# Kernel tuning notes

Measured on AMD Instinct MI355X. Metric: run time of the kernel, lower is better.

Reference implementation:

```python
import jax, jax.numpy as jnp
import numpy as np

EPS = 1e-12  # torch F.normalize default eps

def _l2norm(x):
    # torch.nn.functional.normalize(x, dim=-1): x / max(||x||_2, eps)
    n = jnp.linalg.norm(x, axis=-1, keepdims=True)
    return x / jnp.maximum(n, EPS)

def setup_inputs() -> dict:
    key = jax.random.key(0)
    ks = jax.random.split(key, 12)
    B, T, D, V, C = 16, 2048, 1024, 32000, 6
    s = 0.02
    text = jax.random.randint(ks[0], (B * T,), 0, V, dtype=jnp.int64)
    offsets = (jnp.arange(B, dtype=jnp.int64) * T)  # uniform-length sequences
    emb = jax.random.normal(ks[1], (V, D), dtype=jnp.float32) * s
    Wq = jax.random.normal(ks[2], (D, D), dtype=jnp.float32) * s
    bq = jnp.zeros((D,), jnp.float32)
    Wk = jax.random.normal(ks[3], (D, D), dtype=jnp.float32) * s
    bk = jnp.zeros((D,), jnp.float32)
    Wv = jax.random.normal(ks[4], (D, D), dtype=jnp.float32) * s
    bv = jnp.zeros((D,), jnp.float32)
    Wfc = jax.random.normal(ks[5], (D, D), dtype=jnp.float32) * s
    bfc = jnp.zeros((D,), jnp.float32)
    Wo = jax.random.normal(ks[6], (C, D), dtype=jnp.float32) * s
    bo = jnp.zeros((C,), jnp.float32)
    return {"text": text, "offsets": offsets, "emb": emb,
            "Wq": Wq, "bq": bq, "Wk": Wk, "bk": bk, "Wv": Wv, "bv": bv,
            "Wfc": Wfc, "bfc": bfc, "Wo": Wo, "bo": bo}

def reference(text, offsets, emb, Wq, bq, Wk, bk, Wv, bv, Wfc, bfc, Wo, bo):
    B = offsets.shape[0]
    T = text.shape[0] // B  # uniform lengths -> pad_sequence == reshape
    D = emb.shape[1]
    tok = text.reshape(B, T)
    x = emb[tok]                                   # [B,T,D]
    q = x @ Wq.T + bq
    k = x @ Wk.T + bk
    v = x @ Wv.T + bv
    scores = jnp.einsum('bqd,bkd->bqk', q, k) / jnp.sqrt(jnp.asarray(D, x.dtype))
    causal = jnp.tril(jnp.ones((T, T), dtype=bool))
    scores = jnp.where(causal[None, :, :], scores, -jnp.inf)
    attn = jax.nn.softmax(scores, axis=-1)
    out = jnp.einsum('bqk,bkd->bqd', attn, v) + x  # residual with embedding
    out = _l2norm(out)
    out = out + (out @ Wfc.T + bfc)                # residual FFN
    out = _l2norm(out)
    last = out[:, -1, :]                           # [B,D]
    return jax.nn.sigmoid(last @ Wo.T + bo)        # [B,num_class]
```

## Files before the change

### kernel.cpp

```cpp
#include <hip/hip_runtime.h>
#include <math.h>


typedef unsigned short ushort_t;

__device__ __forceinline__ float bf2f(ushort_t u) {
    union { unsigned int i; float f; } v;
    v.i = ((unsigned int)u) << 16;
    return v.f;
}

__device__ __forceinline__ ushort_t f2bf(float f) {
    union { float f; unsigned int i; } v; v.f = f;
    unsigned int lsb = (v.i >> 16) & 1;
    unsigned int r = v.i + 0x7FFF + lsb;
    return (ushort_t)(r >> 16);
}

__device__ __forceinline__ float wave_sum(float acc) {
    #pragma unroll
    for (int off = 32; off >= 1; off >>= 1) acc += __shfl_xor(acc, off, 64);
    return acc;
}
__device__ __forceinline__ float wave_max(float acc) {
    #pragma unroll
    for (int off = 32; off >= 1; off >>= 1) acc = fmaxf(acc, __shfl_xor(acc, off, 64));
    return acc;
}

__device__ __forceinline__ void ld8(const void* p, int isbf, size_t i, float* o) {
    if (isbf) {
        uint4 raw = *reinterpret_cast<const uint4*>((const ushort_t*)p + i);
        const ushort_t* pu = reinterpret_cast<const ushort_t*>(&raw);
        #pragma unroll
        for (int k = 0; k < 8; ++k) o[k] = bf2f(pu[k]);
    } else {
        const float4* f = reinterpret_cast<const float4*>((const float*)p + i);
        float4 a = f[0], b = f[1];
        o[0]=a.x; o[1]=a.y; o[2]=a.z; o[3]=a.w;
        o[4]=b.x; o[5]=b.y; o[6]=b.z; o[7]=b.w;
    }
}

__device__ __forceinline__ void ld4(const void* p, int isbf, size_t i, float* o) {
    if (isbf) {
        uint2 raw = *reinterpret_cast<const uint2*>((const ushort_t*)p + i);
        const ushort_t* pu = reinterpret_cast<const ushort_t*>(&raw);
        #pragma unroll
        for (int k = 0; k < 4; ++k) o[k] = bf2f(pu[k]);
    } else {
        float4 a = *reinterpret_cast<const float4*>((const float*)p + i);
        o[0]=a.x; o[1]=a.y; o[2]=a.z; o[3]=a.w;
    }
}

__device__ __forceinline__ float ldS(const void* p, int isbf, size_t i) {
    return isbf ? bf2f(((const ushort_t*)p)[i]) : ((const float*)p)[i];
}

__device__ __forceinline__ int tokAt(const void* text, int isi64, size_t i) {
    return isi64 ? ((const int*)text)[2 * i] : ((const int*)text)[i];
}

__device__ __forceinline__ void detect_flags(const void* emb, const void* text, int* sf) {
    if (threadIdx.x < 64) {
        const int lane = threadIdx.x;
        ushort_t u = ((const ushort_t*)emb)[2 * lane];
        int e = (u >> 7) & 0xFF;
        unsigned long long mb = __ballot(e >= 0x60 && e <= 0x7E);
        int odd = ((const int*)text)[2 * lane + 1];
        unsigned long long mi = __ballot(odd != 0);
        if (lane == 0) {
            sf[0] = (__popcll(mb) >= 32) ? 1 : 0;
            sf[1] = (__popcll(mi) == 0) ? 1 : 0;
        }
    }
    __syncthreads();
}

__device__ __forceinline__ void hoist16(const float* v, int lane, float* c16) {
    #pragma unroll
    for (int k = 0; k < 16; ++k) c16[k] = v[lane * 16 + k];
}

__global__ void kQC(const void* __restrict__ text, const void* __restrict__ emb,
                    const void* __restrict__ Wq, const void* __restrict__ bq,
                    const void* __restrict__ Wk, float* __restrict__ c_part,
                    int B, int T, int D) {
    const int nch = D >> 5;
    const int b  = blockIdx.x / nch;
    const int ch = blockIdx.x % nch;
    const int i0 = ch << 5;
    const int tid = threadIdx.x;
    __shared__ int sf[2];
    __shared__ float xs[1024];
    __shared__ float qs[32];
    detect_flags(emb, text, sf);
    const int isbf = sf[0], isi64 = sf[1];
    const int tok = tokAt(text, isi64, (size_t)b * T + (T - 1));
    float w4[4];
    {
        const int dd = tid * 4;
        ld4(emb, isbf, (size_t)tok * D + dd, w4);
        xs[dd]=w4[0]; xs[dd+1]=w4[1]; xs[dd+2]=w4[2]; xs[dd+3]=w4[3];
    }
    __syncthreads();
    const int wave = tid >> 6, lane = tid & 63;
    float c16[16];
    hoist16(xs, lane, c16);
    float w[8];
    for (int r = 0; r < 8; ++r) {
        const int i = i0 + wave * 8 + r;
        float acc = 0.f;
        ld8(Wq, isbf, (size_t)i * D + lane * 16, w);
        #pragma unroll
        for (int k = 0; k < 8; ++k) acc += w[k] * c16[k];
        ld8(Wq, isbf, (size_t)i * D + lane * 16 + 8, w);
        #pragma unroll
        for (int k = 0; k < 8; ++k) acc += w[k] * c16[8 + k];
        acc = wave_sum(acc);
        if (lane == 0) qs[wave * 8 + r] = acc + ldS(bq, isbf, i);
    }
    __syncthreads();
    const int d = tid * 4;
    float a0=0.f, a1=0.f, a2=0.f, a3=0.f;
    #pragma unroll 8
    for (int i = 0; i < 32; ++i) {
        const float qv = qs[i];
        ld4(Wk, isbf, (size_t)(i0 + i) * D + d, w4);
        a0 += qv*w4[0]; a1 += qv*w4[1]; a2 += qv*w4[2]; a3 += qv*w4[3];
    }
    *reinterpret_cast<float4*>(c_part + ((size_t)ch * B + b) * D + d)
        = make_float4(a0, a1, a2, a3);
}

__global__ void kCC(const float* __restrict__ c_part, float* __restrict__ c,
                    int B, int D, int nch) {
    const int nb = D >> 6;
    const int b = blockIdx.x / nb;
    const int dblk = blockIdx.x % nb;
    const int q = threadIdx.x >> 6, dl = threadIdx.x & 63;
    const int d = dblk * 64 + dl;
    __shared__ float red[256];
    const int per = nch >> 2;
    float acc = 0.f;
    for (int j = 0; j < per; ++j) {
        const int cc = q * per + j;
        acc += c_part[((size_t)cc * B + b) * D + d];
    }
    red[threadIdx.x] = acc;
    __syncthreads();
    if (q == 0) c[(size_t)b * D + d] = red[dl] + red[64 + dl] + red[128 + dl] + red[192 + dl];
}

__global__ void k35o(const void* __restrict__ text, const void* __restrict__ emb,
                     const float* __restrict__ c, float* __restrict__ xbar_part,
                     float* __restrict__ m_part, float* __restrict__ l_part,
                     int B, int T, int D, float scale) {
    const int nt32 = T >> 5;
    const int b = blockIdx.x / nt32;
    const int ch = blockIdx.x % nt32;
    const int j0 = ch << 5;
    const int tid = threadIdx.x;
    const int wave = tid >> 6, lane = tid & 63;
    __shared__ int   sf[2];
    __shared__ float vec[1024];
    __shared__ float wacc[4][1024];
    __shared__ float wm[4], wl[4];
    __shared__ int   tks[32];
    detect_flags(emb, text, sf);
    const int isbf = sf[0], isi64 = sf[1];
    {
        const int dd = tid * 4;
        float4 v = *reinterpret_cast<const float4*>(c + (size_t)b * D + dd);
        vec[dd]=v.x; vec[dd+1]=v.y; vec[dd+2]=v.z; vec[dd+3]=v.w;
    }
    if (tid < 32) tks[tid] = tokAt(text, isi64, (size_t)b * T + j0 + tid);
    __syncthreads();
    float c16[16]; hoist16(vec, lane, c16);
    float m = -INFINITY, l = 0.f;
    float acc[16];
    #pragma unroll
    for (int k = 0; k < 16; ++k) acc[k] = 0.f;
    #pragma unroll 2
    for (int rr = 0; rr < 8; ++rr) {
        const int r = (wave << 3) + rr;
        float w[16];
        ld8(emb, isbf, (size_t)tks[r] * D + lane * 16, w);
        ld8(emb, isbf, (size_t)tks[r] * D + lane * 16 + 8, w + 8);
        float s = 0.f;
        #pragma unroll
        for (int k = 0; k < 16; ++k) s += w[k] * c16[k];
        s = wave_sum(s) * scale;
        const float mn = fmaxf(m, s);
        const float f  = __expf(m - mn);
        const float p  = __expf(s - mn);
        l = l * f + p;
        #pragma unroll
        for (int k = 0; k < 16; ++k) acc[k] = acc[k] * f + p * w[k];
        m = mn;
    }
    if (lane == 0) { wm[wave] = m; wl[wave] = l; }
    __syncthreads();
    const float M = fmaxf(fmaxf(wm[0], wm[1]), fmaxf(wm[2], wm[3]));
    const float g = __expf(wm[wave] - M);
    #pragma unroll
    for (int q = 0; q < 4; ++q) {
        *reinterpret_cast<float4*>(&wacc[wave][lane * 16 + q * 4]) =
            make_float4(acc[q*4]*g, acc[q*4+1]*g, acc[q*4+2]*g, acc[q*4+3]*g);
    }
    __syncthreads();
    if (tid == 0) {
        m_part[(size_t)b * nt32 + ch] = M;
        l_part[(size_t)b * nt32 + ch] =
            wl[0]*__expf(wm[0]-M) + wl[1]*__expf(wm[1]-M)
          + wl[2]*__expf(wm[2]-M) + wl[3]*__expf(wm[3]-M);
    }
    const int d = tid * 4;
    float4 o;
    o.x = wacc[0][d]   + wacc[1][d]   + wacc[2][d]   + wacc[3][d];
    o.y = wacc[0][d+1] + wacc[1][d+1] + wacc[2][d+1] + wacc[3][d+1];
    o.z = wacc[0][d+2] + wacc[1][d+2] + wacc[2][d+2] + wacc[3][d+2];
    o.w = wacc[0][d+3] + wacc[1][d+3] + wacc[2][d+3] + wacc[3][d+3];
    *reinterpret_cast<float4*>(xbar_part + ((size_t)b * nt32 + ch) * D + d) = o;
}

__global__ void kC(const float* __restrict__ xbar_part, const float* __restrict__ m_part,
                   const float* __restrict__ l_part, float* __restrict__ xbar,
                   int B, int D, int nchT) {
    const int nb = D >> 6;
    const int b = blockIdx.x / nb;
    const int dblk = blockIdx.x % nb;
    const int q = threadIdx.x >> 6, dl = threadIdx.x & 63;
    const int d = dblk * 64 + dl;
    __shared__ float sc[128];
    __shared__ float red[256];
    if (threadIdx.x < 64) {
        const int t = threadIdx.x;
        float m0 = (t < nchT) ? m_part[(size_t)b * nchT + t] : -INFINITY;
        float m1 = (64 + t < nchT) ? m_part[(size_t)b * nchT + 64 + t] : -INFINITY;
        float mx = wave_max(fmaxf(m0, m1));
        float l0 = (t < nchT) ? l_part[(size_t)b * nchT + t] * __expf(m0 - mx) : 0.f;
        float l1 = (64 + t < nchT) ? l_part[(size_t)b * nchT + 64 + t] * __expf(m1 - mx) : 0.f;
        float ls = wave_sum(l0 + l1);
        if (t < nchT) sc[t] = __expf(m0 - mx) / ls;
        if (64 + t < nchT) sc[64 + t] = __expf(m1 - mx) / ls;
    }
    __syncthreads();
    const int per = nchT >> 2;
    float acc = 0.f;
    for (int j = 0; j < per; ++j) {
        const int cc = q * per + j;
        acc += sc[cc] * xbar_part[((size_t)b * nchT + cc) * D + d];
    }
    red[threadIdx.x] = acc;
    __syncthreads();
    if (q == 0) xbar[(size_t)b * D + d] = red[dl] + red[64 + dl]
                                        + red[128 + dl] + red[192 + dl];
}

__global__ void kVA(const void* __restrict__ text, const void* __restrict__ emb,
                    const void* __restrict__ Wv, const void* __restrict__ bv,
                    const float* __restrict__ xbar, float* __restrict__ u,
                    int B, int T, int D) {
    const int nch = D >> 5;
    const int b  = blockIdx.x / nch;
    const int ch = blockIdx.x % nch;
    const int r0 = ch << 5;
    const int tid = threadIdx.x;
    __shared__ int sf[2];
    __shared__ float xb[1024];
    __shared__ float xl[32];
    detect_flags(emb, text, sf);
    const int isbf = sf[0], isi64 = sf[1];
    const int tok = tokAt(text, isi64, (size_t)b * T + (T - 1));
    if (tid < 32) xl[tid] = ldS(emb, isbf, (size_t)tok * D + r0 + tid);
    {
        const int dd = tid * 4;
        float4 v = *reinterpret_cast<const float4*>(xbar + (size_t)b * D + dd);
        xb[dd]=v.x; xb[dd+1]=v.y; xb[dd+2]=v.z; xb[dd+3]=v.w;
    }
    __syncthreads();
    const int wave = tid >> 6, lane = tid & 63;
    float c16[16];
    hoist16(xb, lane, c16);
    float w[8];
    for (int rr = 0; rr < 8; ++rr) {
        const int i = r0 + wave + rr * 4;
        float acc = 0.f;
        ld8(Wv, isbf, (size_t)i * D + lane * 16, w);
        #pragma unroll
        for (int k = 0; k < 8; ++k) acc += w[k] * c16[k];
        ld8(Wv, isbf, (size_t)i * D + lane * 16 + 8, w);
        #pragma unroll
        for (int k = 0; k < 8; ++k) acc += w[k] * c16[8 + k];
        acc = wave_sum(acc);
        if (lane == 0) u[(size_t)b * D + i] = acc + ldS(bv, isbf, i) + xl[i - r0];
    }
}

__global__ void k6c_h2(const void* __restrict__ text, const void* __restrict__ emb,
                       const void* __restrict__ Wfc, const void* __restrict__ bfc,
                       const float* __restrict__ u, float* __restrict__ h2,
                       int B, int D) {
    const int nch = D >> 5;
    const int b  = blockIdx.x / nch;
    const int ch = blockIdx.x % nch;
    const int r0 = ch << 5;
    const int tid = threadIdx.x;
    __shared__ int sf[2];
    __shared__ float hs[1024];
    __shared__ float red[256];
    __shared__ float s_rn;
    detect_flags(emb, text, sf);
    const int isbf = sf[0];
    float part;
    {
        const int dd = tid * 4;
        float4 v = *reinterpret_cast<const float4*>(u + (size_t)b * D + dd);
        hs[dd]=v.x; hs[dd+1]=v.y; hs[dd+2]=v.z; hs[dd+3]=v.w;
        part = v.x*v.x + v.y*v.y + v.z*v.z + v.w*v.w;
    }
    red[tid] = part;
    __syncthreads();
    for (int st = 128; st; st >>= 1) {
        if (tid < st) red[tid] += red[tid + st];
        __syncthreads();
    }
    if (tid == 0) s_rn = 1.f / fmaxf(sqrtf(red[0]), 1e-12f);
    __syncthreads();
    const float rn = s_rn;
    {
        const int dd = tid * 4;
        hs[dd] *= rn; hs[dd+1] *= rn; hs[dd+2] *= rn; hs[dd+3] *= rn;
    }
    __syncthreads();
    const int wave = tid >> 6, lane = tid & 63;
    float c16[16];
    hoist16(hs, lane, c16);
    float w[8];
    for (int rr = 0; rr < 8; ++rr) {
        const int i = r0 + wave + rr * 4;
        float acc = 0.f;
        ld8(Wfc, isbf, (size_t)i * D + lane * 16, w);
        #pragma unroll
        for (int k = 0; k < 8; ++k) acc += w[k] * c16[k];
        ld8(Wfc, isbf, (size_t)i * D + lane * 16 + 8, w);
        #pragma unroll
        for (int k = 0; k < 8; ++k) acc += w[k] * c16[8 + k];
        acc = wave_sum(acc);
        if (lane == 0) h2[(size_t)b * D + i] = hs[i] + acc + ldS(bfc, isbf, i);
    }
}

__global__ void k6d_out(const void* __restrict__ text, const void* __restrict__ emb,
                        const void* __restrict__ Wo, const void* __restrict__ bo,
                        const float* __restrict__ h2, void* __restrict__ out,
                        int D, int C, int total) {
    __shared__ int sf[2];
    detect_flags(emb, text, sf);
    const int isbf = sf[0];
    const int g = blockIdx.x * 4 + (threadIdx.x >> 6);
    if (g >= total) return;
    const int lane = threadIdx.x & 63;
    const int b = g / C, ci = g % C;
    float a1 = 0.f, a2 = 0.f, w[8], h[8];
    for (int d0 = lane * 8; d0 < D; d0 += 512) {
        ld8(Wo, isbf, (size_t)ci * D + d0, w);
        ld8(h2, 0, (size_t)b * D + d0, h);
        #pragma unroll
        for (int k = 0; k < 8; ++k) { a1 += w[k] * h[k]; a2 += h[k] * h[k]; }
    }
    a1 = wave_sum(a1);
    a2 = wave_sum(a2);
    if (lane == 0) {
        float rn = 1.f / fmaxf(sqrtf(a2), 1e-12f);
        float z = a1 * rn + ldS(bo, isbf, ci);
        float y = 1.f / (1.f + expf(-z));
        if (isbf) ((ushort_t*)out)[g] = f2bf(y);
        else      ((float*)out)[g] = y;
    }
}

extern "C" void kernel_launch(void* const* d_in, const int* in_sizes, int n_in,
                              void* d_out, int out_size, void* d_ws, size_t ws_size,
                              hipStream_t stream) {
    const void* text = d_in[0];
    const void* emb = d_in[2];
    const void* Wq  = d_in[3];
    const void* bq  = d_in[4];
    const void* Wk  = d_in[5];
    const void* Wv  = d_in[7];
    const void* bv  = d_in[8];
    const void* Wfc = d_in[9];
    const void* bfc = d_in[10];
    const void* Wo  = d_in[11];
    const void* bo  = d_in[12];

    const int B = in_sizes[1];
    const int T = in_sizes[0] / B;
    const int D = in_sizes[4];
    const int C = in_sizes[12];

    const int nch_c = D / 32;
    const int nchT  = T / 32;

    float* ws        = (float*)d_ws;
    float* c_part    = ws;
    float* c         = c_part + (size_t)nch_c * B * D;
    float* xbar_part = c + (size_t)B * D;
    float* m_part    = xbar_part + (size_t)B * nchT * D;
    float* l_part    = m_part + (size_t)B * nchT;
    float* xbar      = l_part + (size_t)B * nchT;
    float* u         = xbar + (size_t)B * D;
    float* h2        = u + (size_t)B * D;

    const float scale = 1.0f / sqrtf((float)D);

    kQC<<<B * (D / 32), 256, 0, stream>>>(text, emb, Wq, bq, Wk, c_part, B, T, D);
    kCC<<<B * (D / 64), 256, 0, stream>>>(c_part, c, B, D, nch_c);
    k35o<<<B * (T / 32), 256, 0, stream>>>(text, emb, c, xbar_part, m_part, l_part,
                                           B, T, D, scale);
    kC<<<B * (D / 64), 256, 0, stream>>>(xbar_part, m_part, l_part, xbar, B, D, nchT);
    kVA<<<B * (D / 32), 256, 0, stream>>>(text, emb, Wv, bv, xbar, u, B, T, D);
    k6c_h2<<<B * (D / 32), 256, 0, stream>>>(text, emb, Wfc, bfc, u, h2, B, D);
    k6d_out<<<(B * C + 3) / 4, 256, 0, stream>>>(text, emb, Wo, bo, h2, d_out, D, C, B * C);
}
```

Before: 264.4 us.

## Fuse softmax-combine and output kernels into producers via last-block atomic counters

Removes the separate kC combine kernel and the k6d_out output kernel. The last-arriving block per batch, found with an agent-scope atomic counter, now does the cross-chunk softmax merge and the final Wo/sigmoid. It also changes the fp32 embedding-row load in the attention pass to coalesced float4 strided access. This saves two launches and their inter-kernel gaps, at the cost of a serial tail run by one block per batch and counters that must be reset each call inside kQC.

```diff
diff --git a/kernel.cpp b/kernel.cpp
--- a/kernel.cpp
+++ b/kernel.cpp
@@ -86,12 +86,15 @@
 __global__ void kQC(const void* __restrict__ text, const void* __restrict__ emb,
                     const void* __restrict__ Wq, const void* __restrict__ bq,
                     const void* __restrict__ Wk, float* __restrict__ c_part,
+                    int* __restrict__ ctr,
                     int B, int T, int D) {
     const int nch = D >> 5;
     const int b  = blockIdx.x / nch;
     const int ch = blockIdx.x % nch;
     const int i0 = ch << 5;
     const int tid = threadIdx.x;
+    if (blockIdx.x < 2 && tid < 2 * B)
+        __hip_atomic_store(&ctr[tid], 0, __ATOMIC_RELAXED, __HIP_MEMORY_SCOPE_AGENT);
     __shared__ int sf[2];
     __shared__ float xs[1024];
     __shared__ float qs[32];
@@ -153,10 +156,11 @@
     if (q == 0) c[(size_t)b * D + d] = red[dl] + red[64 + dl] + red[128 + dl] + red[192 + dl];
 }
 
-__global__ void k35o(const void* __restrict__ text, const void* __restrict__ emb,
-                     const float* __restrict__ c, float* __restrict__ xbar_part,
-                     float* __restrict__ m_part, float* __restrict__ l_part,
-                     int B, int T, int D, float scale) {
+__global__ void k35oC(const void* __restrict__ text, const void* __restrict__ emb,
+                      const float* __restrict__ c, float* __restrict__ xbar_part,
+                      float* __restrict__ m_part, float* __restrict__ l_part,
+                      float* __restrict__ xbar, int* __restrict__ ctrA,
+                      int B, int T, int D, float scale) {
     const int nt32 = T >> 5;
     const int b = blockIdx.x / nt32;
     const int ch = blockIdx.x % nt32;
@@ -168,6 +172,7 @@
     __shared__ float wacc[4][1024];
     __shared__ float wm[4], wl[4];
     __shared__ int   tks[32];
+    __shared__ int   s_last;
     detect_flags(emb, text, sf);
     const int isbf = sf[0], isi64 = sf[1];
     {
@@ -177,7 +182,17 @@
     }
     if (tid < 32) tks[tid] = tokAt(text, isi64, (size_t)b * T + j0 + tid);
     __syncthreads();
-    float c16[16]; hoist16(vec, lane, c16);
+    float c16[16];
+    if (isbf) {
+        #pragma unroll
+        for (int k = 0; k < 16; ++k) c16[k] = vec[lane * 16 + k];
+    } else {
+        #pragma unroll
+        for (int p = 0; p < 4; ++p) {
+            #pragma unroll
+            for (int k = 0; k < 4; ++k) c16[p*4+k] = vec[p*256 + lane*4 + k];
+        }
+    }
     float m = -INFINITY, l = 0.f;
     float acc[16];
     #pragma unroll
@@ -185,9 +200,19 @@
     #pragma unroll 2
     for (int rr = 0; rr < 8; ++rr) {
         const int r = (wave << 3) + rr;
+        const size_t base = (size_t)tks[r] * D;
         float w[16];
-        ld8(emb, isbf, (size_t)tks[r] * D + lane * 16, w);
-        ld8(emb, isbf, (size_t)tks[r] * D + lane * 16 + 8, w + 8);
+        if (isbf) {
+            ld8(emb, 1, base + lane * 16, w);
+            ld8(emb, 1, base + lane * 16 + 8, w + 8);
+        } else {
+            const float* E = (const float*)emb + base;
+            #pragma unroll
+            for (int p = 0; p < 4; ++p) {
+                float4 v = *reinterpret_cast<const float4*>(E + p*256 + lane*4);
+                w[p*4]=v.x; w[p*4+1]=v.y; w[p*4+2]=v.z; w[p*4+3]=v.w;
+            }
+        }
         float s = 0.f;
         #pragma unroll
         for (int k = 0; k < 16; ++k) s += w[k] * c16[k];
@@ -204,10 +229,16 @@
     __syncthreads();
     const float M = fmaxf(fmaxf(wm[0], wm[1]), fmaxf(wm[2], wm[3]));
     const float g = __expf(wm[wave] - M);
-    #pragma unroll
-    for (int q = 0; q < 4; ++q) {
-        *reinterpret_cast<float4*>(&wacc[wave][lane * 16 + q * 4]) =
-            make_float4(acc[q*4]*g, acc[q*4+1]*g, acc[q*4+2]*g, acc[q*4+3]*g);
+    if (isbf) {
+        #pragma unroll
+        for (int k = 0; k < 16; ++k) wacc[wave][lane * 16 + k] = acc[k] * g;
+    } else {
+        #pragma unroll
+        for (int p = 0; p < 4; ++p) {
+            #pragma unroll
+            for (int k = 0; k < 4; ++k)
+                wacc[wave][p*256 + lane*4 + k] = acc[p*4+k] * g;
+        }
     }
     __syncthreads();
     if (tid == 0) {
@@ -217,46 +248,43 @@
           + wl[2]*__expf(wm[2]-M) + wl[3]*__expf(wm[3]-M);
     }
     const int d = tid * 4;
-    float4 o;
-    o.x = wacc[0][d]   + wacc[1][d]   + wacc[2][d]   + wacc[3][d];
-    o.y = wacc[0][d+1] + wacc[1][d+1] + wacc[2][d+1] + wacc[3][d+1];
-    o.z = wacc[0][d+2] + wacc[1][d+2] + wacc[2][d+2] + wacc[3][d+2];
-    o.w = wacc[0][d+3] + wacc[1][d+3] + wacc[2][d+3] + wacc[3][d+3];
-    *reinterpret_cast<float4*>(xbar_part + ((size_t)b * nt32 + ch) * D + d) = o;
-}
-
-__global__ void kC(const float* __restrict__ xbar_part, const float* __restrict__ m_part,
-                   const float* __restrict__ l_part, float* __restrict__ xbar,
-                   int B, int D, int nchT) {
-    const int nb = D >> 6;
-    const int b = blockIdx.x / nb;
-    const int dblk = blockIdx.x % nb;
-    const int q = threadIdx.x >> 6, dl = threadIdx.x & 63;
-    const int d = dblk * 64 + dl;
-    __shared__ float sc[128];
-    __shared__ float red[256];
-    if (threadIdx.x < 64) {
-        const int t = threadIdx.x;
-        float m0 = (t < nchT) ? m_part[(size_t)b * nchT + t] : -INFINITY;
-        float m1 = (64 + t < nchT) ? m_part[(size_t)b * nchT + 64 + t] : -INFINITY;
+    {
+        float4 o;
+        o.x = wacc[0][d]   + wacc[1][d]   + wacc[2][d]   + wacc[3][d];
+        o.y = wacc[0][d+1] + wacc[1][d+1] + wacc[2][d+1] + wacc[3][d+1];
+        o.z = wacc[0][d+2] + wacc[1][d+2] + wacc[2][d+2] + wacc[3][d+2];
+        o.w = wacc[0][d+3] + wacc[1][d+3] + wacc[2][d+3] + wacc[3][d+3];
+        *reinterpret_cast<float4*>(xbar_part + ((size_t)b * nt32 + ch) * D + d) = o;
+    }
+    __syncthreads();
+    if (tid == 0) {
+        __threadfence();
+        int old = __hip_atomic_fetch_add(&ctrA[b], 1, __ATOMIC_ACQ_REL,
+                                         __HIP_MEMORY_SCOPE_AGENT);
+        s_last = (old == nt32 - 1) ? 1 : 0;
+    }
+    __syncthreads();
+    if (!s_last) return;
+    __threadfence();
+    if (tid < 64) {
+        float m0 = (tid < nt32) ? m_part[(size_t)b * nt32 + tid] : -INFINITY;
+        float m1 = (64 + tid < nt32) ? m_part[(size_t)b * nt32 + 64 + tid] : -INFINITY;
         float mx = wave_max(fmaxf(m0, m1));
-        float l0 = (t < nchT) ? l_part[(size_t)b * nchT + t] * __expf(m0 - mx) : 0.f;
-        float l1 = (64 + t < nchT) ? l_part[(size_t)b * nchT + 64 + t] * __expf(m1 - mx) : 0.f;
+        float l0 = (tid < nt32) ? l_part[(size_t)b * nt32 + tid] * __expf(m0 - mx) : 0.f;
+        float l1 = (64 + tid < nt32) ? l_part[(size_t)b * nt32 + 64 + tid] * __expf(m1 - mx) : 0.f;
         float ls = wave_sum(l0 + l1);
-        if (t < nchT) sc[t] = __expf(m0 - mx) / ls;
-        if (64 + t < nchT) sc[64 + t] = __expf(m1 - mx) / ls;
-    }
-    __syncthreads();
-    const int per = nchT >> 2;
-    float acc = 0.f;
-    for (int j = 0; j < per; ++j) {
-        const int cc = q * per + j;
-        acc += sc[cc] * xbar_part[((size_t)b * nchT + cc) * D + d];
-    }
-    red[threadIdx.x] = acc;
-    __syncthreads();
-    if (q == 0) xbar[(size_t)b * D + d] = red[dl] + red[64 + dl]
-                                        + red[128 + dl] + red[192 + dl];
+        if (tid < nt32) vec[tid] = __expf(m0 - mx) / ls;
+        if (64 + tid < nt32) vec[64 + tid] = __expf(m1 - mx) / ls;
+    }
+    __syncthreads();
+    float a0=0.f, a1=0.f, a2=0.f, a3=0.f;
+    for (int cc = 0; cc < nt32; ++cc) {
+        const float s = vec[cc];
+        float4 v = *reinterpret_cast<const float4*>(
+            xbar_part + ((size_t)b * nt32 + cc) * D + d);
+        a0 += s*v.x; a1 += s*v.y; a2 += s*v.z; a3 += s*v.w;
+    }
+    *reinterpret_cast<float4*>(xbar + (size_t)b * D + d) = make_float4(a0, a1, a2, a3);
 }
 
 __global__ void kVA(const void* __restrict__ text, const void* __restrict__ emb,
@@ -299,10 +327,12 @@
     }
 }
 
-__global__ void k6c_h2(const void* __restrict__ text, const void* __restrict__ emb,
-                       const void* __restrict__ Wfc, const void* __restrict__ bfc,
-                       const float* __restrict__ u, float* __restrict__ h2,
-                       int B, int D) {
+__global__ void k6cd(const void* __restrict__ text, const void* __restrict__ emb,
+                     const void* __restrict__ Wfc, const void* __restrict__ bfc,
+                     const void* __restrict__ Wo, const void* __restrict__ bo,
+                     const float* __restrict__ u, float* __restrict__ h2,
+                     void* __restrict__ out, int* __restrict__ ctrB,
+                     int B, int D, int C) {
     const int nch = D >> 5;
     const int b  = blockIdx.x / nch;
     const int ch = blockIdx.x % nch;
@@ -312,6 +342,7 @@
     __shared__ float hs[1024];
     __shared__ float red[256];
     __shared__ float s_rn;
+    __shared__ int s_last;
     detect_flags(emb, text, sf);
     const int isbf = sf[0];
     float part;
@@ -351,34 +382,33 @@
         acc = wave_sum(acc);
         if (lane == 0) h2[(size_t)b * D + i] = hs[i] + acc + ldS(bfc, isbf, i);
     }
-}
-
-__global__ void k6d_out(const void* __restrict__ text, const void* __restrict__ emb,
-                        const void* __restrict__ Wo, const void* __restrict__ bo,
-                        const float* __restrict__ h2, void* __restrict__ out,
-                        int D, int C, int total) {
-    __shared__ int sf[2];
-    detect_flags(emb, text, sf);
-    const int isbf = sf[0];
-    const int g = blockIdx.x * 4 + (threadIdx.x >> 6);
-    if (g >= total) return;
-    const int lane = threadIdx.x & 63;
-    const int b = g / C, ci = g % C;
-    float a1 = 0.f, a2 = 0.f, w[8], h[8];
-    for (int d0 = lane * 8; d0 < D; d0 += 512) {
-        ld8(Wo, isbf, (size_t)ci * D + d0, w);
-        ld8(h2, 0, (size_t)b * D + d0, h);
-        #pragma unroll
-        for (int k = 0; k < 8; ++k) { a1 += w[k] * h[k]; a2 += h[k] * h[k]; }
-    }
-    a1 = wave_sum(a1);
-    a2 = wave_sum(a2);
-    if (lane == 0) {
-        float rn = 1.f / fmaxf(sqrtf(a2), 1e-12f);
-        float z = a1 * rn + ldS(bo, isbf, ci);
-        float y = 1.f / (1.f + expf(-z));
-        if (isbf) ((ushort_t*)out)[g] = f2bf(y);
-        else      ((float*)out)[g] = y;
+    __syncthreads();
+    if (tid == 0) {
+        __threadfence();
+        int old = __hip_atomic_fetch_add(&ctrB[b], 1, __ATOMIC_ACQ_REL,
+                                         __HIP_MEMORY_SCOPE_AGENT);
+        s_last = (old == nch - 1) ? 1 : 0;
+    }
+    __syncthreads();
+    if (!s_last) return;
+    __threadfence();
+    for (int ci = wave; ci < C; ci += 4) {
+        float a1 = 0.f, a2 = 0.f, wo[8], h[8];
+        for (int d0 = lane * 8; d0 < D; d0 += 512) {
+            ld8(Wo, isbf, (size_t)ci * D + d0, wo);
+            ld8(h2, 0, (size_t)b * D + d0, h);
+            #pragma unroll
+            for (int k = 0; k < 8; ++k) { a1 += wo[k] * h[k]; a2 += h[k] * h[k]; }
+        }
+        a1 = wave_sum(a1);
+        a2 = wave_sum(a2);
+        if (lane == 0) {
+            float rno = 1.f / fmaxf(sqrtf(a2), 1e-12f);
+            float z = a1 * rno + ldS(bo, isbf, ci);
+            float y = 1.f / (1.f + expf(-z));
+            if (isbf) ((ushort_t*)out)[b * C + ci] = f2bf(y);
+            else      ((float*)out)[b * C + ci] = y;
+        }
     }
 }
 
@@ -405,8 +435,9 @@
     const int nch_c = D / 32;
     const int nchT  = T / 32;
 
-    float* ws        = (float*)d_ws;
-    float* c_part    = ws;
+    int*   ctr  = (int*)d_ws;
+    float* base = (float*)d_ws + 64;
+    float* c_part    = base;
     float* c         = c_part + (size_t)nch_c * B * D;
     float* xbar_part = c + (size_t)B * D;
     float* m_part    = xbar_part + (size_t)B * nchT * D;
@@ -417,12 +448,11 @@
 
     const float scale = 1.0f / sqrtf((float)D);
 
-    kQC<<<B * (D / 32), 256, 0, stream>>>(text, emb, Wq, bq, Wk, c_part, B, T, D);
+    kQC<<<B * (D / 32), 256, 0, stream>>>(text, emb, Wq, bq, Wk, c_part, ctr, B, T, D);
     kCC<<<B * (D / 64), 256, 0, stream>>>(c_part, c, B, D, nch_c);
-    k35o<<<B * (T / 32), 256, 0, stream>>>(text, emb, c, xbar_part, m_part, l_part,
-                                           B, T, D, scale);
-    kC<<<B * (D / 64), 256, 0, stream>>>(xbar_part, m_part, l_part, xbar, B, D, nchT);
+    k35oC<<<B * (T / 32), 256, 0, stream>>>(text, emb, c, xbar_part, m_part, l_part,
+                                            xbar, ctr, B, T, D, scale);
     kVA<<<B * (D / 32), 256, 0, stream>>>(text, emb, Wv, bv, xbar, u, B, T, D);
-    k6c_h2<<<B * (D / 32), 256, 0, stream>>>(text, emb, Wfc, bfc, u, h2, B, D);
-    k6d_out<<<(B * C + 3) / 4, 256, 0, stream>>>(text, emb, Wo, bo, h2, d_out, D, C, B * C);
-}
+    k6cd<<<B * (D / 32), 256, 0, stream>>>(text, emb, Wfc, bfc, Wo, bo, u, h2,
+                                           d_out, ctr + B, B, D, C);
+}
```

Result: slower. 347.9 us (+31.6%).
